# Kernel tuning notes

Hardware: AMD Instinct MI355X
Metric: run time of the kernel (lower is better)

## Reference

```python
import jax, jax.numpy as jnp
import numpy as np

# Dimensions
B, T, H = 4, 4096, 2048          # batch, seq, hidden
NH = 16                           # total hash heads = (max_ngram-1)*n_head_per_ngram
PER_HEAD_VOCAB = 100000
DH = 64                           # per-head embedding dim
E = NH * DH                       # engram_hidden_size = 1024
G = 4                             # hc_mult
K = 4                             # kernel_size
DIL = 3                           # dilation = max_ngram_size
EPS_RMS = 1.1920929e-07           # torch RMSNorm default eps (fp32 finfo eps)
EPS_SC = 1e-5                     # ShortConv RMSNorm eps


def setup_inputs() -> dict:
    key = jax.random.key(0)
    ks = jax.random.split(key, 12)
    hidden_states = jax.random.normal(ks[0], (T, B, H), dtype=jnp.float32)
    hash_ids = jax.random.randint(ks[1], (B, T, NH), 0, PER_HEAD_VOCAB)
    emb_table = jax.random.normal(ks[2], (NH * PER_HEAD_VOCAB, DH), dtype=jnp.float32)
    s = 0.02
    key_W = jax.random.normal(ks[3], (G, H, E), dtype=jnp.float32) * s
    key_b = jax.random.normal(ks[4], (G, H), dtype=jnp.float32) * s
    value_W = jax.random.normal(ks[5], (H, E), dtype=jnp.float32) * s
    value_b = jax.random.normal(ks[6], (H,), dtype=jnp.float32) * s
    norm1_w = jnp.ones((G, H), dtype=jnp.float32)
    norm2_w = jnp.ones((G, H), dtype=jnp.float32)
    sc_norm_w = jnp.ones((G, H), dtype=jnp.float32)
    conv_w = jax.random.normal(ks[7], (G * H, K), dtype=jnp.float32) * 0.1
    return {"hidden_states": hidden_states, "hash_ids": hash_ids, "emb_table": emb_table,
            "key_W": key_W, "key_b": key_b, "value_W": value_W, "value_b": value_b,
            "norm1_w": norm1_w, "norm2_w": norm2_w, "sc_norm_w": sc_norm_w, "conv_w": conv_w}


def _rms(x, eps):
    return x * jax.lax.rsqrt(jnp.mean(x * x, axis=-1, keepdims=True) + eps)


def reference(hidden_states, hash_ids, emb_table, key_W, key_b, value_W, value_b,
              norm1_w, norm2_w, sc_norm_w, conv_w):
    # --- precompute_embeddings: hashed multi-head gather ---
    offsets = jnp.arange(NH, dtype=hash_ids.dtype) * PER_HEAD_VOCAB
    emb = emb_table[hash_ids + offsets]              # [B,T,NH,DH]
    emb = emb.reshape(B, T, E)                       # [B,T,E]

    # --- forward ---
    hs = jnp.transpose(hidden_states, (1, 0, 2))     # [B,T,H]
    # per-group key projection + RMSNorm (vectorized over G)
    keys = jnp.einsum('bte,ghe->btgh', emb, key_W) + key_b   # [B,T,G,H]
    nk = _rms(keys, EPS_RMS) * norm1_w               # [B,T,G,H]
    nq = _rms(hs, EPS_RMS)[:, :, None, :] * norm2_w  # [B,T,G,H]
    gate = jnp.sum(nk * nq, axis=-1) / np.sqrt(H)    # [B,T,G]
    gate = jnp.sqrt(jnp.maximum(jnp.abs(gate), 1e-6)) * jnp.sign(gate)
    gate = jax.nn.sigmoid(gate)[..., None]           # [B,T,G,1]
    value = gate * (emb @ value_W.T + value_b)[:, :, None, :]   # [B,T,G,H]

    # --- ShortConv: per-group RMSNorm -> causal dilated depthwise conv -> SiLU ---
    xn = _rms(value, EPS_SC) * sc_norm_w             # [B,T,G,H]
    x_bct = xn.reshape(B, T, G * H).transpose(0, 2, 1)  # [B,G*H,T]
    y = jax.lax.conv_general_dilated(
        x_bct, conv_w[:, None, :],                   # rhs [C,1,K]
        window_strides=(1,), padding=[((K - 1) * DIL, 0)],
        rhs_dilation=(DIL,), dimension_numbers=('NCH', 'OIH', 'NCH'),
        feature_group_count=G * H)                   # [B,G*H,T]
    y = jax.nn.silu(y)
    y = y.transpose(0, 2, 1).reshape(B, T, G, H)

    out = (value + y).mean(axis=2)                   # [B,T,H]
    return jnp.transpose(out, (1, 0, 2))             # [S,B,H]
```

## Files before the change

### kernel.cpp

```cpp
#include <hip/hip_runtime.h>
#include <hip/hip_bf16.h>

#define BB 4
#define TT 4096
#define HH 2048
#define NHH 16
#define VOC 100000
#define EE 1024
#define GG 4
#define BT (BB*TT)
#define NKEY (GG*HH)
#define NTOT (NKEY+HH)
#define NPART 32
#define TCV 48

static constexpr float EPS_RMS = 1.1920929e-07f;
static constexpr float EPS_SC  = 1e-5f;
static constexpr float INV_SQRT_H = 0.02209708691207961f;

using f32x4 = __attribute__((ext_vector_type(4))) float;
using f32x2 = __attribute__((ext_vector_type(2))) float;
using s8v   = __attribute__((ext_vector_type(8))) short;
using gvoid = __attribute__((address_space(1))) const void;
using lvoid = __attribute__((address_space(3))) void;

__device__ __forceinline__ unsigned short f2bf(float f){
  union { __hip_bfloat16 h; unsigned short u; } cv;
  cv.h = __float2bfloat16(f);
  return cv.u;
}
__device__ __forceinline__ float bf2f(unsigned short u){
  union { float f; unsigned u; } cv;
  cv.u = ((unsigned)u) << 16;
  return cv.f;
}

__global__ __launch_bounds__(256) void convw_kern(const float* __restrict__ kW,
    const float* __restrict__ vW, unsigned short* __restrict__ Wc){
  const long idx  = (long)blockIdx.x*256 + threadIdx.x;
  const long base = idx*4;
  const long KN   = (long)NKEY*EE;
  float4 v;
  if (base < KN) v = *(const float4*)(kW + base);
  else           v = *(const float4*)(vW + (base - KN));
  ushort4 o; o.x=f2bf(v.x); o.y=f2bf(v.y); o.z=f2bf(v.z); o.w=f2bf(v.w);
  *(ushort4*)(Wc + base) = o;
}

__global__ __launch_bounds__(256) void prep_kern(const int* __restrict__ hids,
    const float* __restrict__ table, unsigned short* __restrict__ emb,
    const float* __restrict__ hs, float* __restrict__ rq,
    unsigned short* __restrict__ hsbf){
  const int p = blockIdx.x, tid = threadIdx.x;
  const int e = tid*4, head = e>>6, d = e&63;
  const long row = (long)hids[p*NHH + head] + (long)head*VOC;
  const float4 v = *(const float4*)(table + row*64 + d);
  ushort4 o; o.x=f2bf(v.x); o.y=f2bf(v.y); o.z=f2bf(v.z); o.w=f2bf(v.w);
  *(ushort4*)(emb + (size_t)p*EE + e) = o;
  const int b = p>>12, t = p&4095;
  const float* hrow = hs + ((size_t)t*BB + b)*HH;
  const int e8 = tid*8;
  float4 v0 = *(const float4*)(hrow+e8);
  float4 v1 = *(const float4*)(hrow+e8+4);
  ushort4 hb0; hb0.x=f2bf(v0.x); hb0.y=f2bf(v0.y); hb0.z=f2bf(v0.z); hb0.w=f2bf(v0.w);
  ushort4 hb1; hb1.x=f2bf(v1.x); hb1.y=f2bf(v1.y); hb1.z=f2bf(v1.z); hb1.w=f2bf(v1.w);
  *(ushort4*)(hsbf + (size_t)p*HH + e8)     = hb0;
  *(ushort4*)(hsbf + (size_t)p*HH + e8 + 4) = hb1;
  float s = v0.x*v0.x+v0.y*v0.y+v0.z*v0.z+v0.w*v0.w
          + v1.x*v1.x+v1.y*v1.y+v1.z*v1.z+v1.w*v1.w;
  #pragma unroll
  for (int of=32;of>=1;of>>=1) s += __shfl_xor(s,of);
  __shared__ float red[4];
  if ((tid&63)==0) red[tid>>6] = s;
  __syncthreads();
  if (tid==0){
    float tot = red[0]+red[1]+red[2]+red[3];
    rq[p] = rsqrtf(tot*(1.0f/HH) + EPS_RMS);
  }
}

__global__ __launch_bounds__(512, 2) void gemm8(
    const unsigned short* __restrict__ A, const unsigned short* __restrict__ Bw,
    const float* __restrict__ key_b, const float* __restrict__ value_b,
    const float* __restrict__ n1w, const float* __restrict__ n2w,
    const unsigned short* __restrict__ hsbf, unsigned short* __restrict__ vlinb,
    f32x2* __restrict__ sdp, float* __restrict__ vsqp)
{
  __shared__ unsigned short sh[65536];
  const int tid = threadIdx.x, w = tid>>6, l = tid&63;
  const int wm = w>>2, wn = w&3;
  const int lg = l&15, lr = l>>4;
  const int wg  = blockIdx.x;
  const int swz = (wg&7)*320 + (wg>>3);
  const int tM  = swz/40, tN = swz - tM*40;
  const int Mrow0 = tM*256, Nrow0 = tN*256;

  const int lp = l>>3, lcs = (l&7)^lp;
  const size_t aoffT = (size_t)(Mrow0 + w*16 + lp)*EE + lcs*8;
  const size_t boffT = (size_t)(Nrow0 + w*16 + lp)*EE + lcs*8;
  const int c0 = lr ^ (lg&7);
  const unsigned aBase = (unsigned)(wm*8192 + lg*64);
  const unsigned bBase = (unsigned)(16384 + (wn>>1)*8192 + (wn&1)*4096 + lg*64);

  f32x4 acc[8][4] = {};
  s8v aR0[4], aR1[4], bR0[4], bR1[4];

#define STAGEH(ISB, H, KT, SB) { \
    const unsigned short* s0_ = ((ISB) ? (Bw + boffT) : (A + aoffT)) + (H)*131072 + (KT)*64; \
    const unsigned d0_ = (SB)*32768 + (ISB)*16384 + (H)*8192 + w*1024; \
    __builtin_amdgcn_global_load_lds((gvoid*)s0_,        (lvoid*)(sh + d0_),       16, 0, 0); \
    __builtin_amdgcn_global_load_lds((gvoid*)(s0_+8192), (lvoid*)(sh + d0_ + 512), 16, 0, 0); \
  }
#define STAGE4(KT, SB) { STAGEH(0,0,KT,SB); STAGEH(0,1,KT,SB); STAGEH(1,0,KT,SB); STAGEH(1,1,KT,SB); }

#define BAR() { asm volatile("" ::: "memory"); __builtin_amdgcn_s_barrier(); asm volatile("" ::: "memory"); }

#define RD_A(CB, KK, MH, DST) { \
    const unsigned short* p_ = sh + (CB)*32768 + aBase; \
    const unsigned ck_ = (unsigned)((c0 ^ ((KK)<<2))<<3); \
    DST[0] = *(const s8v*)(p_ + ((MH)*4+0)*1024 + ck_); \
    DST[1] = *(const s8v*)(p_ + ((MH)*4+1)*1024 + ck_); \
    DST[2] = *(const s8v*)(p_ + ((MH)*4+2)*1024 + ck_); \
    DST[3] = *(const s8v*)(p_ + ((MH)*4+3)*1024 + ck_); }

#define RD_B(CB, KK, DST) { \
    const unsigned short* p_ = sh + (CB)*32768 + bBase; \
    const unsigned ck_ = (unsigned)((c0 ^ ((KK)<<2))<<3); \
    DST[0] = *(const s8v*)(p_ + 0*1024 + ck_); \
    DST[1] = *(const s8v*)(p_ + 1*1024 + ck_); \
    DST[2] = *(const s8v*)(p_ + 2*1024 + ck_); \
    DST[3] = *(const s8v*)(p_ + 3*1024 + ck_); }

#define MM(MH, AF, BF) { \
    __builtin_amdgcn_s_setprio(1); \
    _Pragma("unroll") \
    for (int mf=0; mf<4; mf++) \
      _Pragma("unroll") \
      for (int nf=0; nf<4; nf++) \
        acc[(MH)*4+mf][nf] = __builtin_amdgcn_mfma_f32_16x16x32_bf16(AF[mf], BF[nf], acc[(MH)*4+mf][nf], 0,0,0); \
    __builtin_amdgcn_s_setprio(0); }

#define TILE(CB, NB, KT1, DOST) { \
    BAR(); \
    if (DOST) STAGE4(KT1, NB); \
    RD_A(CB,1,0,aR1); RD_B(CB,1,bR1); \
    MM(0, aR0, bR0); \
    RD_A(CB,0,1,aR0); \
    MM(0, aR1, bR1); \
    RD_A(CB,1,1,aR1); \
    MM(1, aR0, bR0); \
    asm volatile("s_waitcnt vmcnt(0)" ::: "memory"); \
    BAR(); \
    RD_A(NB,0,0,aR0); RD_B(NB,0,bR0); \
    MM(1, aR1, bR1); }

#define TILE_LAST(CB) { \
    BAR(); \
    RD_A(CB,1,0,aR1); RD_B(CB,1,bR1); \
    MM(0, aR0, bR0); \
    RD_A(CB,0,1,aR0); \
    MM(0, aR1, bR1); \
    RD_A(CB,1,1,aR1); \
    MM(1, aR0, bR0); \
    MM(1, aR1, bR1); }

  STAGE4(0, 0);
  asm volatile("s_waitcnt vmcnt(0)" ::: "memory");
  BAR();
  RD_A(0,0,0,aR0); RD_B(0,0,bR0);

  #pragma unroll 1
  for (int i=0; i<7; i++){
    const int kt = 2*i;
    TILE(0, 1, kt+1, true);
    TILE(1, 0, kt+2, true);
  }
  TILE(0, 1, 15, true);
  TILE_LAST(1);

#undef STAGEH
#undef STAGE4
#undef RD_A
#undef RD_B
#undef MM
#undef TILE
#undef TILE_LAST

  BAR();

  const bool isK = (Nrow0 < NKEY);
  float bias[4], cw[4]; int hcol[4];
  #pragma unroll
  for (int nf=0; nf<4; nf++){
    const int n = Nrow0 + wn*64 + nf*16 + lg;
    hcol[nf] = n & (HH-1);
    if (isK){ bias[nf] = key_b[n]; cw[nf] = n1w[n]*n2w[n]; }
    else    { bias[nf] = value_b[n-NKEY]; cw[nf] = 0.f; }
  }

  if (isK){
    const int g = Nrow0 >> 11;
    const int slot = (tN&7)*4 + wn;
    char* wreg = (char*)sh + w*16384;
    #pragma unroll
    for (int mfa=0; mfa<8; mfa++){
      #pragma unroll
      for (int rr=0; rr<4; rr++){
        const int rowl = mfa*16 + lr*4 + rr;
        const int p = Mrow0 + wm*128 + rowl;
        const unsigned short* hrow = hsbf + (size_t)p*HH;
        float ssq=0.f, dt=0.f;
        #pragma unroll
        for (int nf=0; nf<4; nf++){
          const float c = acc[mfa][nf][rr] + bias[nf];
          ssq += c*c;
          dt  += c * cw[nf] * bf2f(hrow[hcol[nf]]);
        }
        f32x2 pr; pr[0]=ssq; pr[1]=dt;
        *(f32x2*)(wreg + rowl*128 + (((lg>>1) ^ (rowl&7))<<4) + ((lg&1)<<3)) = pr;
      }
    }
    #pragma unroll
    for (int rh=0; rh<2; rh++){
      const int r = l + rh*64;
      float ssq=0.f, dt=0.f;
      #pragma unroll
      for (int c=0; c<8; c++){
        f32x4 v = *(const f32x4*)(wreg + r*128 + ((c ^ (r&7))<<4));
        ssq += v[0] + v[2]; dt += v[1] + v[3];
      }
      const int p = Mrow0 + wm*128 + r;
      f32x2 o; o[0]=ssq; o[1]=dt;
      sdp[(size_t)(p*GG+g)*NPART + slot] = o;
    }
  } else {
    const int slot = (tN-32)*4 + wn;
    const int h0 = Nrow0 - NKEY + wn*64;
    const int pbase = Mrow0 + wm*128;
    #pragma unroll
    for (int mfa=0; mfa<8; mfa++){
      #pragma unroll
      for (int rr=0; rr<4; rr++){
        const int p = pbase + mfa*16 + lr*4 + rr;
        float ssq=0.f;
        #pragma unroll
        for (int nf=0; nf<4; nf++){
          const float c = acc[mfa][nf][rr] + bias[nf];
          vlinb[(size_t)p*HH + h0 + nf*16 + lg] = f2bf(c);
          ssq += c*c;
        }
        #pragma unroll
        for (int o=1;o<16;o<<=1){ ssq += __shfl_xor(ssq,o); }
        if (lg==0) vsqp[(size_t)p*NPART + slot] = ssq;
      }
    }
  }
}

__global__ __launch_bounds__(256) void scal_kern(const f32x2* __restrict__ sdp,
    const float* __restrict__ vsqp,
    const float* __restrict__ rq, float* __restrict__ gate, float* __restrict__ av){
  const int i = blockIdx.x*256 + threadIdx.x;
  const int p = i>>2;
  float ss=0.f, dd=0.f, vv=0.f;
  const f32x2* sp = sdp + (size_t)i*NPART;
  #pragma unroll
  for (int j=0;j<NPART;j++){ f32x2 v = sp[j]; ss += v[0]; dd += v[1]; }
  #pragma unroll
  for (int j=0;j<NPART;j++){ vv += vsqp[(size_t)p*NPART+j]; }
  const float rk = rsqrtf(ss*(1.0f/HH) + EPS_RMS);
  const float gv = rk * rq[p] * dd * INV_SQRT_H;
  const float sgn = (gv>0.f)?1.f:((gv<0.f)?-1.f:0.f);
  const float g1 = sqrtf(fmaxf(fabsf(gv),1e-6f))*sgn;
  const float gt = 1.f/(1.f+__expf(-g1));
  const float msvl = vv*(1.0f/HH);
  const float a = gt * rsqrtf(gt*gt*msvl + EPS_SC);
  gate[i]=gt; av[i]=a;
}

__device__ __forceinline__ ushort4 ldrow(const unsigned short* __restrict__ v, int b, int t, int h0){
  if (t < 0){ ushort4 z; z.x=0;z.y=0;z.z=0;z.w=0; return z; }
  return *(const ushort4*)(v + (size_t)((b<<12)|t)*HH + h0);
}
__device__ __forceinline__ void ldav(const float* __restrict__ av, int b, int t, float* a){
  if (t < 0){ a[0]=0.f;a[1]=0.f;a[2]=0.f;a[3]=0.f; }
  else { const float4 x = *(const float4*)(av + (size_t)((b<<12)|t)*GG);
         a[0]=x.x;a[1]=x.y;a[2]=x.z;a[3]=x.w; }
}

__global__ __launch_bounds__(256) void conv2_kern(const unsigned short* __restrict__ vlinb,
    const float* __restrict__ gate, const float* __restrict__ av,
    const float* __restrict__ conv_w, const float* __restrict__ scw,
    float* __restrict__ out){
  const int bx = blockIdx.x;
  const int b  = blockIdx.y;
  const int t0 = (bx>>1)*TCV;
  const int h0 = (bx&1)*1024 + threadIdx.x*4;

  float cwv[4][4][4];
  float sc4[4][4];
  #pragma unroll
  for (int g=0; g<4; g++){
    #pragma unroll
    for (int j2=0; j2<4; j2++){
      const int c = g*HH + h0 + j2;
      const float4 wv = *(const float4*)(conv_w + (size_t)c*4);
      cwv[g][j2][0]=wv.x; cwv[g][j2][1]=wv.y; cwv[g][j2][2]=wv.z; cwv[g][j2][3]=wv.w;
      sc4[g][j2] = scw[c];
    }
  }

  #pragma unroll 1
  for (int r=0; r<3; r++){
    const int tf = t0 + r;
    ushort4 w0 = ldrow(vlinb, b, tf-9, h0);
    ushort4 w1 = ldrow(vlinb, b, tf-6, h0);
    ushort4 w2 = ldrow(vlinb, b, tf-3, h0);
    ushort4 w3; w3.x=0;w3.y=0;w3.z=0;w3.w=0;
    #pragma unroll
    for (int j=0; j<16; j++){
      const int t = tf + 3*j;
      if (t < TT){
        const int p = (b<<12)|t;
        w3 = *(const ushort4*)(vlinb + (size_t)p*HH + h0);
        float a0[4],a1[4],a2[4],a3[4];
        ldav(av, b, t-9, a0); ldav(av, b, t-6, a1); ldav(av, b, t-3, a2); ldav(av, b, t, a3);
        float gt4[4];
        { const float4 x = *(const float4*)(gate + (size_t)p*GG);
          gt4[0]=x.x; gt4[1]=x.y; gt4[2]=x.z; gt4[3]=x.w; }
        float v0[4],v1[4],v2[4],v3[4];
        v0[0]=bf2f(w0.x); v0[1]=bf2f(w0.y); v0[2]=bf2f(w0.z); v0[3]=bf2f(w0.w);
        v1[0]=bf2f(w1.x); v1[1]=bf2f(w1.y); v1[2]=bf2f(w1.z); v1[3]=bf2f(w1.w);
        v2[0]=bf2f(w2.x); v2[1]=bf2f(w2.y); v2[2]=bf2f(w2.z); v2[3]=bf2f(w2.w);
        v3[0]=bf2f(w3.x); v3[1]=bf2f(w3.y); v3[2]=bf2f(w3.z); v3[3]=bf2f(w3.w);
        float4 ov;
        float res[4];
        #pragma unroll
        for (int j2=0; j2<4; j2++){
          float acc = 0.f;
          #pragma unroll
          for (int g=0; g<4; g++){
            float y = cwv[g][j2][0]*a0[g]*v0[j2]
                    + cwv[g][j2][1]*a1[g]*v1[j2]
                    + cwv[g][j2][2]*a2[g]*v2[j2]
                    + cwv[g][j2][3]*a3[g]*v3[j2];
            y *= sc4[g][j2];
            const float sy = y * (1.f/(1.f+__expf(-y)));
            acc += gt4[g]*v3[j2] + sy;
          }
          res[j2] = acc*0.25f;
        }
        ov.x=res[0]; ov.y=res[1]; ov.z=res[2]; ov.w=res[3];
        *(float4*)(out + ((size_t)t*BB + b)*HH + h0) = ov;
      }
      w0=w1; w1=w2; w2=w3;
    }
  }
}

extern "C" void kernel_launch(void* const* d_in, const int* in_sizes, int n_in,
                              void* d_out, int out_size, void* d_ws, size_t ws_size,
                              hipStream_t stream){
  (void)in_sizes; (void)n_in; (void)out_size; (void)ws_size;
  const float* hs    = (const float*)d_in[0];
  const int*   hids  = (const int*)d_in[1];
  const float* table = (const float*)d_in[2];
  const float* keyW  = (const float*)d_in[3];
  const float* keyB  = (const float*)d_in[4];
  const float* valW  = (const float*)d_in[5];
  const float* valB  = (const float*)d_in[6];
  const float* n1w   = (const float*)d_in[7];
  const float* n2w   = (const float*)d_in[8];
  const float* scw   = (const float*)d_in[9];
  const float* convw = (const float*)d_in[10];
  float* out = (float*)d_out;

  char* ws = (char*)d_ws;
  size_t off = 0;
  unsigned short* emb   = (unsigned short*)(ws+off); off += (size_t)BT*EE*2;
  unsigned short* Wc    = (unsigned short*)(ws+off); off += (size_t)NTOT*EE*2;
  unsigned short* vlinb = (unsigned short*)(ws+off); off += (size_t)BT*HH*2;
  unsigned short* hsbf  = (unsigned short*)(ws+off); off += (size_t)BT*HH*2;
  f32x2* sdp    = (f32x2*)(ws+off); off += (size_t)BT*GG*NPART*8;
  float* vsqp   = (float*)(ws+off); off += (size_t)BT*NPART*4;
  float* rq     = (float*)(ws+off); off += (size_t)BT*4;
  float* gate   = (float*)(ws+off); off += (size_t)BT*GG*4;
  float* av     = (float*)(ws+off); off += (size_t)BT*GG*4;

  convw_kern<<<(NTOT*EE/4)/256, 256, 0, stream>>>(keyW, valW, Wc);
  prep_kern<<<BT, 256, 0, stream>>>(hids, table, emb, hs, rq, hsbf);
  gemm8<<<2560, 512, 0, stream>>>(emb, Wc, keyB, valB, n1w, n2w, hsbf, vlinb, sdp, vsqp);
  scal_kern<<<(BT*GG)/256, 256, 0, stream>>>(sdp, vsqp, rq, gate, av);
  dim3 cg(((TT + TCV - 1)/TCV)*2, BB);
  conv2_kern<<<cg, 256, 0, stream>>>(vlinb, gate, av, convw, scw, out);
}
```

Baseline: 554.5 us.

## Pre-pack GEMM operands into MFMA fragment layout and load directly to registers

The weight cast and the embedding gather now write A and B in a fragment-major layout. Each lane can then fetch its 16-byte MFMA fragment straight from global memory. This lets the GEMM drop LDS staging, the swizzled LDS reads and the barriers, and use a simple register double-buffered loop. The tile-to-block mapping also changes to a new stripe-based swizzle for L2 locality. The cost is that every wave reissues global loads with no LDS sharing, so the kernel leans more on L2 bandwidth and latency hiding from two blocks per CU. The 128KB LDS array is still reserved for the epilogue.

```diff
diff --git a/kernel.cpp b/kernel.cpp
--- a/kernel.cpp
+++ b/kernel.cpp
@@ -21,8 +21,6 @@
 using f32x4 = __attribute__((ext_vector_type(4))) float;
 using f32x2 = __attribute__((ext_vector_type(2))) float;
 using s8v   = __attribute__((ext_vector_type(8))) short;
-using gvoid = __attribute__((address_space(1))) const void;
-using lvoid = __attribute__((address_space(3))) void;
 
 __device__ __forceinline__ unsigned short f2bf(float f){
   union { __hip_bfloat16 h; unsigned short u; } cv;
@@ -34,38 +32,56 @@
   cv.u = ((unsigned)u) << 16;
   return cv.f;
 }
-
-__global__ __launch_bounds__(256) void convw_kern(const float* __restrict__ kW,
-    const float* __restrict__ vW, unsigned short* __restrict__ Wc){
-  const long idx  = (long)blockIdx.x*256 + threadIdx.x;
-  const long base = idx*4;
-  const long KN   = (long)NKEY*EE;
-  float4 v;
-  if (base < KN) v = *(const float4*)(kW + base);
-  else           v = *(const float4*)(vW + (base - KN));
-  ushort4 o; o.x=f2bf(v.x); o.y=f2bf(v.y); o.z=f2bf(v.z); o.w=f2bf(v.w);
-  *(ushort4*)(Wc + base) = o;
-}
-
-__global__ __launch_bounds__(256) void prep_kern(const int* __restrict__ hids,
-    const float* __restrict__ table, unsigned short* __restrict__ emb,
-    const float* __restrict__ hs, float* __restrict__ rq,
-    unsigned short* __restrict__ hsbf){
+__device__ __forceinline__ s8v pack8(float4 v0, float4 v1){
+  s8v o;
+  o[0]=(short)f2bf(v0.x); o[1]=(short)f2bf(v0.y); o[2]=(short)f2bf(v0.z); o[3]=(short)f2bf(v0.w);
+  o[4]=(short)f2bf(v1.x); o[5]=(short)f2bf(v1.y); o[6]=(short)f2bf(v1.z); o[7]=(short)f2bf(v1.w);
+  return o;
+}
+
+__global__ __launch_bounds__(256) void convw_pack(const float* __restrict__ kW,
+    const float* __restrict__ vW, unsigned short* __restrict__ Bpk){
+  const int nb = blockIdx.x;
+  const int t = threadIdx.x, lane = t&63, q = t>>6;
+  const int n = nb*16 + (lane&15);
+  const float* src = (n < NKEY) ? (kW + (size_t)n*EE) : (vW + (size_t)(n-NKEY)*EE);
+  #pragma unroll
+  for (int i=0;i<8;i++){
+    const int kb = q*8 + i;
+    const int k0 = kb*32 + (lane>>4)*8;
+    float4 v0 = *(const float4*)(src + k0);
+    float4 v1 = *(const float4*)(src + k0 + 4);
+    *(s8v*)(Bpk + (size_t)(nb*32 + kb)*512 + lane*8) = pack8(v0, v1);
+  }
+}
+
+__global__ __launch_bounds__(256) void prep_pack(const int* __restrict__ hids,
+    const float* __restrict__ table, unsigned short* __restrict__ Apk){
+  const int pb = blockIdx.x;
+  const int t = threadIdx.x, lane = t&63, q = t>>6;
+  const int p = pb*16 + (lane&15);
+  #pragma unroll
+  for (int i=0;i<8;i++){
+    const int kb = q*8 + i;
+    const int k0 = kb*32 + (lane>>4)*8;
+    const int head = k0>>6;
+    const long row = (long)hids[p*NHH + head] + (long)head*VOC;
+    const float* src = table + row*64 + (k0&63);
+    float4 v0 = *(const float4*)(src);
+    float4 v1 = *(const float4*)(src + 4);
+    *(s8v*)(Apk + (size_t)(pb*32 + kb)*512 + lane*8) = pack8(v0, v1);
+  }
+}
+
+__global__ __launch_bounds__(256) void prep_hs(const float* __restrict__ hs,
+    float* __restrict__ rq, unsigned short* __restrict__ hsbf){
   const int p = blockIdx.x, tid = threadIdx.x;
-  const int e = tid*4, head = e>>6, d = e&63;
-  const long row = (long)hids[p*NHH + head] + (long)head*VOC;
-  const float4 v = *(const float4*)(table + row*64 + d);
-  ushort4 o; o.x=f2bf(v.x); o.y=f2bf(v.y); o.z=f2bf(v.z); o.w=f2bf(v.w);
-  *(ushort4*)(emb + (size_t)p*EE + e) = o;
   const int b = p>>12, t = p&4095;
   const float* hrow = hs + ((size_t)t*BB + b)*HH;
   const int e8 = tid*8;
   float4 v0 = *(const float4*)(hrow+e8);
   float4 v1 = *(const float4*)(hrow+e8+4);
-  ushort4 hb0; hb0.x=f2bf(v0.x); hb0.y=f2bf(v0.y); hb0.z=f2bf(v0.z); hb0.w=f2bf(v0.w);
-  ushort4 hb1; hb1.x=f2bf(v1.x); hb1.y=f2bf(v1.y); hb1.z=f2bf(v1.z); hb1.w=f2bf(v1.w);
-  *(ushort4*)(hsbf + (size_t)p*HH + e8)     = hb0;
-  *(ushort4*)(hsbf + (size_t)p*HH + e8 + 4) = hb1;
+  *(s8v*)(hsbf + (size_t)p*HH + e8) = pack8(v0, v1);
   float s = v0.x*v0.x+v0.y*v0.y+v0.z*v0.z+v0.w*v0.w
           + v1.x*v1.x+v1.y*v1.y+v1.z*v1.z+v1.w*v1.w;
   #pragma unroll
@@ -79,114 +95,58 @@
   }
 }
 
-__global__ __launch_bounds__(512, 2) void gemm8(
-    const unsigned short* __restrict__ A, const unsigned short* __restrict__ Bw,
+__global__ __launch_bounds__(512, 2) void gemm(
+    const unsigned short* __restrict__ Apk, const unsigned short* __restrict__ Bpk,
     const float* __restrict__ key_b, const float* __restrict__ value_b,
     const float* __restrict__ n1w, const float* __restrict__ n2w,
     const unsigned short* __restrict__ hsbf, unsigned short* __restrict__ vlinb,
     f32x2* __restrict__ sdp, float* __restrict__ vsqp)
 {
-  __shared__ unsigned short sh[65536];
+  __shared__ char sh[131072];
   const int tid = threadIdx.x, w = tid>>6, l = tid&63;
   const int wm = w>>2, wn = w&3;
   const int lg = l&15, lr = l>>4;
-  const int wg  = blockIdx.x;
-  const int swz = (wg&7)*320 + (wg>>3);
-  const int tM  = swz/40, tN = swz - tM*40;
+  const int wg = blockIdx.x;
+  const int x = wg&7, lid = wg>>3;
+  const int stripe = lid/160, rr0 = lid - stripe*160;
+  const int tN = rr0>>2, tM = x*8 + stripe*4 + (rr0&3);
   const int Mrow0 = tM*256, Nrow0 = tN*256;
 
-  const int lp = l>>3, lcs = (l&7)^lp;
-  const size_t aoffT = (size_t)(Mrow0 + w*16 + lp)*EE + lcs*8;
-  const size_t boffT = (size_t)(Nrow0 + w*16 + lp)*EE + lcs*8;
-  const int c0 = lr ^ (lg&7);
-  const unsigned aBase = (unsigned)(wm*8192 + lg*64);
-  const unsigned bBase = (unsigned)(16384 + (wn>>1)*8192 + (wn&1)*4096 + lg*64);
+  unsigned aof[8], bof[4];
+  #pragma unroll
+  for (int mf=0;mf<8;mf++) aof[mf] = (unsigned)((tM*16 + wm*8 + mf)*32)*512u + (unsigned)l*8u;
+  #pragma unroll
+  for (int nf=0;nf<4;nf++) bof[nf] = (unsigned)((tN*16 + wn*4 + nf)*32)*512u + (unsigned)l*8u;
 
   f32x4 acc[8][4] = {};
-  s8v aR0[4], aR1[4], bR0[4], bR1[4];
-
-#define STAGEH(ISB, H, KT, SB) { \
-    const unsigned short* s0_ = ((ISB) ? (Bw + boffT) : (A + aoffT)) + (H)*131072 + (KT)*64; \
-    const unsigned d0_ = (SB)*32768 + (ISB)*16384 + (H)*8192 + w*1024; \
-    __builtin_amdgcn_global_load_lds((gvoid*)s0_,        (lvoid*)(sh + d0_),       16, 0, 0); \
-    __builtin_amdgcn_global_load_lds((gvoid*)(s0_+8192), (lvoid*)(sh + d0_ + 512), 16, 0, 0); \
-  }
-#define STAGE4(KT, SB) { STAGEH(0,0,KT,SB); STAGEH(0,1,KT,SB); STAGEH(1,0,KT,SB); STAGEH(1,1,KT,SB); }
-
-#define BAR() { asm volatile("" ::: "memory"); __builtin_amdgcn_s_barrier(); asm volatile("" ::: "memory"); }
-
-#define RD_A(CB, KK, MH, DST) { \
-    const unsigned short* p_ = sh + (CB)*32768 + aBase; \
-    const unsigned ck_ = (unsigned)((c0 ^ ((KK)<<2))<<3); \
-    DST[0] = *(const s8v*)(p_ + ((MH)*4+0)*1024 + ck_); \
-    DST[1] = *(const s8v*)(p_ + ((MH)*4+1)*1024 + ck_); \
-    DST[2] = *(const s8v*)(p_ + ((MH)*4+2)*1024 + ck_); \
-    DST[3] = *(const s8v*)(p_ + ((MH)*4+3)*1024 + ck_); }
-
-#define RD_B(CB, KK, DST) { \
-    const unsigned short* p_ = sh + (CB)*32768 + bBase; \
-    const unsigned ck_ = (unsigned)((c0 ^ ((KK)<<2))<<3); \
-    DST[0] = *(const s8v*)(p_ + 0*1024 + ck_); \
-    DST[1] = *(const s8v*)(p_ + 1*1024 + ck_); \
-    DST[2] = *(const s8v*)(p_ + 2*1024 + ck_); \
-    DST[3] = *(const s8v*)(p_ + 3*1024 + ck_); }
-
-#define MM(MH, AF, BF) { \
+  s8v aA[8], aB[8], bA[4], bB[4];
+
+#define LDF(DSTA, DSTB, S) { \
+    _Pragma("unroll") \
+    for (int mf_=0;mf_<8;mf_++) DSTA[mf_] = *(const s8v*)(Apk + aof[mf_] + (unsigned)(S)*512u); \
+    _Pragma("unroll") \
+    for (int nf_=0;nf_<4;nf_++) DSTB[nf_] = *(const s8v*)(Bpk + bof[nf_] + (unsigned)(S)*512u); }
+
+#define MMB(AF, BF) { \
     __builtin_amdgcn_s_setprio(1); \
     _Pragma("unroll") \
-    for (int mf=0; mf<4; mf++) \
+    for (int mf_=0;mf_<8;mf_++) \
       _Pragma("unroll") \
-      for (int nf=0; nf<4; nf++) \
-        acc[(MH)*4+mf][nf] = __builtin_amdgcn_mfma_f32_16x16x32_bf16(AF[mf], BF[nf], acc[(MH)*4+mf][nf], 0,0,0); \
+      for (int nf_=0;nf_<4;nf_++) \
+        acc[mf_][nf_] = __builtin_amdgcn_mfma_f32_16x16x32_bf16(AF[mf_], BF[nf_], acc[mf_][nf_], 0,0,0); \
     __builtin_amdgcn_s_setprio(0); }
 
-#define TILE(CB, NB, KT1, DOST) { \
-    BAR(); \
-    if (DOST) STAGE4(KT1, NB); \
-    RD_A(CB,1,0,aR1); RD_B(CB,1,bR1); \
-    MM(0, aR0, bR0); \
-    RD_A(CB,0,1,aR0); \
-    MM(0, aR1, bR1); \
-    RD_A(CB,1,1,aR1); \
-    MM(1, aR0, bR0); \
-    asm volatile("s_waitcnt vmcnt(0)" ::: "memory"); \
-    BAR(); \
-    RD_A(NB,0,0,aR0); RD_B(NB,0,bR0); \
-    MM(1, aR1, bR1); }
-
-#define TILE_LAST(CB) { \
-    BAR(); \
-    RD_A(CB,1,0,aR1); RD_B(CB,1,bR1); \
-    MM(0, aR0, bR0); \
-    RD_A(CB,0,1,aR0); \
-    MM(0, aR1, bR1); \
-    RD_A(CB,1,1,aR1); \
-    MM(1, aR0, bR0); \
-    MM(1, aR1, bR1); }
-
-  STAGE4(0, 0);
-  asm volatile("s_waitcnt vmcnt(0)" ::: "memory");
-  BAR();
-  RD_A(0,0,0,aR0); RD_B(0,0,bR0);
-
+  LDF(aA, bA, 0);
   #pragma unroll 1
-  for (int i=0; i<7; i++){
-    const int kt = 2*i;
-    TILE(0, 1, kt+1, true);
-    TILE(1, 0, kt+2, true);
-  }
-  TILE(0, 1, 15, true);
-  TILE_LAST(1);
-
-#undef STAGEH
-#undef STAGE4
-#undef RD_A
-#undef RD_B
-#undef MM
-#undef TILE
-#undef TILE_LAST
-
-  BAR();
+  for (int s=0; s<32; s+=2){
+    LDF(aB, bB, s+1);
+    MMB(aA, bA);
+    const int s2 = (s+2 < 32) ? s+2 : 31;
+    LDF(aA, bA, s2);
+    MMB(aB, bB);
+  }
+#undef LDF
+#undef MMB
 
   const bool isK = (Nrow0 < NKEY);
   float bias[4], cw[4]; int hcol[4];
@@ -201,7 +161,7 @@
   if (isK){
     const int g = Nrow0 >> 11;
     const int slot = (tN&7)*4 + wn;
-    char* wreg = (char*)sh + w*16384;
+    char* wreg = sh + w*16384;
     #pragma unroll
     for (int mfa=0; mfa<8; mfa++){
       #pragma unroll
@@ -326,8 +286,8 @@
         float a0[4],a1[4],a2[4],a3[4];
         ldav(av, b, t-9, a0); ldav(av, b, t-6, a1); ldav(av, b, t-3, a2); ldav(av, b, t, a3);
         float gt4[4];
-        { const float4 x = *(const float4*)(gate + (size_t)p*GG);
-          gt4[0]=x.x; gt4[1]=x.y; gt4[2]=x.z; gt4[3]=x.w; }
+        { const float4 xx = *(const float4*)(gate + (size_t)p*GG);
+          gt4[0]=xx.x; gt4[1]=xx.y; gt4[2]=xx.z; gt4[3]=xx.w; }
         float v0[4],v1[4],v2[4],v3[4];
         v0[0]=bf2f(w0.x); v0[1]=bf2f(w0.y); v0[2]=bf2f(w0.z); v0[3]=bf2f(w0.w);
         v1[0]=bf2f(w1.x); v1[1]=bf2f(w1.y); v1[2]=bf2f(w1.z); v1[3]=bf2f(w1.w);
@@ -377,8 +337,8 @@
 
   char* ws = (char*)d_ws;
   size_t off = 0;
-  unsigned short* emb   = (unsigned short*)(ws+off); off += (size_t)BT*EE*2;
-  unsigned short* Wc    = (unsigned short*)(ws+off); off += (size_t)NTOT*EE*2;
+  unsigned short* Apk   = (unsigned short*)(ws+off); off += (size_t)BT*EE*2;
+  unsigned short* Bpk   = (unsigned short*)(ws+off); off += (size_t)NTOT*EE*2;
   unsigned short* vlinb = (unsigned short*)(ws+off); off += (size_t)BT*HH*2;
   unsigned short* hsbf  = (unsigned short*)(ws+off); off += (size_t)BT*HH*2;
   f32x2* sdp    = (f32x2*)(ws+off); off += (size_t)BT*GG*NPART*8;
@@ -387,9 +347,10 @@
   float* gate   = (float*)(ws+off); off += (size_t)BT*GG*4;
   float* av     = (float*)(ws+off); off += (size_t)BT*GG*4;
 
-  convw_kern<<<(NTOT*EE/4)/256, 256, 0, stream>>>(keyW, valW, Wc);
-  prep_kern<<<BT, 256, 0, stream>>>(hids, table, emb, hs, rq, hsbf);
-  gemm8<<<2560, 512, 0, stream>>>(emb, Wc, keyB, valB, n1w, n2w, hsbf, vlinb, sdp, vsqp);
+  convw_pack<<<NTOT/16, 256, 0, stream>>>(keyW, valW, Bpk);
+  prep_pack<<<BT/16, 256, 0, stream>>>(hids, table, Apk);
+  prep_hs<<<BT, 256, 0, stream>>>(hs, rq, hsbf);
+  gemm<<<2560, 512, 0, stream>>>(Apk, Bpk, keyB, valB, n1w, n2w, hsbf, vlinb, sdp, vsqp);
   scal_kern<<<(BT*GG)/256, 256, 0, stream>>>(sdp, vsqp, rq, gate, av);
   dim3 cg(((TT + TCV - 1)/TCV)*2, BB);
   conv2_kern<<<cg, 256, 0, stream>>>(vlinb, gate, av, convw, scw, out);
```

After: 697.4 us. 1.26x slower.

## Triple-buffer GEMM LDS pipeline with half-depth K tiles and rolling conv scale registers

Applied to the files above, without the earlier changes.

The bf16 MFMA GEMM main loop moves from a double-buffered 64-wide K tile to a triple-buffered 32-wide K tile. Two stages are prefetched ahead and waits use a partial vmcnt, so global-to-LDS loads overlap more MFMA work. LDS is enlarged to 96KB and the swizzle and fragment read layout are reworked, which may reduce occupancy at 2 blocks per CU. The key epilogue is split into two halves to fit the smaller per-wave scratch. The conv kernel keeps the scale factors for earlier timesteps in registers and rotates them instead of reloading four per step.

```diff
diff --git a/kernel.cpp b/kernel.cpp
--- a/kernel.cpp
+++ b/kernel.cpp
@@ -86,7 +86,7 @@
     const unsigned short* __restrict__ hsbf, unsigned short* __restrict__ vlinb,
     f32x2* __restrict__ sdp, float* __restrict__ vsqp)
 {
-  __shared__ unsigned short sh[65536];
+  __shared__ char sh[98304];
   const int tid = threadIdx.x, w = tid>>6, l = tid&63;
   const int wm = w>>2, wn = w&3;
   const int lg = l&15, lr = l>>4;
@@ -95,98 +95,96 @@
   const int tM  = swz/40, tN = swz - tM*40;
   const int Mrow0 = tM*256, Nrow0 = tN*256;
 
-  const int lp = l>>3, lcs = (l&7)^lp;
-  const size_t aoffT = (size_t)(Mrow0 + w*16 + lp)*EE + lcs*8;
-  const size_t boffT = (size_t)(Nrow0 + w*16 + lp)*EE + lcs*8;
-  const int c0 = lr ^ (lg&7);
-  const unsigned aBase = (unsigned)(wm*8192 + lg*64);
-  const unsigned bBase = (unsigned)(16384 + (wn>>1)*8192 + (wn&1)*4096 + lg*64);
+  const int srow = l>>2, schunk = (l&3) ^ (srow&3);
+  const size_t aoffS = (size_t)(Mrow0 + w*32 + srow)*EE + schunk*8;
+  const size_t boffS = (size_t)(Nrow0 + w*32 + srow)*EE + schunk*8;
+  const unsigned cSw = (unsigned)((lr ^ (lg&3))<<4);
+  const unsigned aB0 = (unsigned)(wm*8192 + lg*64) + cSw;
+  const unsigned bB0 = 16384u + (unsigned)(wn*4096 + lg*64) + cSw;
 
   f32x4 acc[8][4] = {};
-  s8v aR0[4], aR1[4], bR0[4], bR1[4];
-
-#define STAGEH(ISB, H, KT, SB) { \
-    const unsigned short* s0_ = ((ISB) ? (Bw + boffT) : (A + aoffT)) + (H)*131072 + (KT)*64; \
-    const unsigned d0_ = (SB)*32768 + (ISB)*16384 + (H)*8192 + w*1024; \
-    __builtin_amdgcn_global_load_lds((gvoid*)s0_,        (lvoid*)(sh + d0_),       16, 0, 0); \
-    __builtin_amdgcn_global_load_lds((gvoid*)(s0_+8192), (lvoid*)(sh + d0_ + 512), 16, 0, 0); \
-  }
-#define STAGE4(KT, SB) { STAGEH(0,0,KT,SB); STAGEH(0,1,KT,SB); STAGEH(1,0,KT,SB); STAGEH(1,1,KT,SB); }
+  s8v aF0, aF1, aR2, aR3, aR4, aR5, aR6, aR7;
+  s8v bP[4], bQ[4];
 
 #define BAR() { asm volatile("" ::: "memory"); __builtin_amdgcn_s_barrier(); asm volatile("" ::: "memory"); }
-
-#define RD_A(CB, KK, MH, DST) { \
-    const unsigned short* p_ = sh + (CB)*32768 + aBase; \
-    const unsigned ck_ = (unsigned)((c0 ^ ((KK)<<2))<<3); \
-    DST[0] = *(const s8v*)(p_ + ((MH)*4+0)*1024 + ck_); \
-    DST[1] = *(const s8v*)(p_ + ((MH)*4+1)*1024 + ck_); \
-    DST[2] = *(const s8v*)(p_ + ((MH)*4+2)*1024 + ck_); \
-    DST[3] = *(const s8v*)(p_ + ((MH)*4+3)*1024 + ck_); }
-
-#define RD_B(CB, KK, DST) { \
-    const unsigned short* p_ = sh + (CB)*32768 + bBase; \
-    const unsigned ck_ = (unsigned)((c0 ^ ((KK)<<2))<<3); \
-    DST[0] = *(const s8v*)(p_ + 0*1024 + ck_); \
-    DST[1] = *(const s8v*)(p_ + 1*1024 + ck_); \
-    DST[2] = *(const s8v*)(p_ + 2*1024 + ck_); \
-    DST[3] = *(const s8v*)(p_ + 3*1024 + ck_); }
-
-#define MM(MH, AF, BF) { \
+#define WAITV(N) asm volatile("s_waitcnt vmcnt(" #N ")" ::: "memory")
+
+#define STG(ISB, J, KT, SB) { \
+    const unsigned short* s_ = ((ISB) ? (Bw + boffS) : (A + aoffS)) + (J)*16*EE + (KT)*32; \
+    __builtin_amdgcn_global_load_lds((gvoid*)s_, \
+        (lvoid*)(sh + (SB)*32768 + (ISB)*16384 + w*2048 + (J)*1024), 16, 0, 0); }
+#define STAGE4(KT, SB) { STG(0,0,KT,SB); STG(0,1,KT,SB); STG(1,0,KT,SB); STG(1,1,KT,SB); }
+
+#define RD_A(CB, MF, DST) { DST = *(const s8v*)(sh + (CB)*32768 + aB0 + (MF)*1024); }
+#define RD_B(CB, DSTARR) { \
+    DSTARR[0] = *(const s8v*)(sh + (CB)*32768 + bB0 + 0*1024); \
+    DSTARR[1] = *(const s8v*)(sh + (CB)*32768 + bB0 + 1*1024); \
+    DSTARR[2] = *(const s8v*)(sh + (CB)*32768 + bB0 + 2*1024); \
+    DSTARR[3] = *(const s8v*)(sh + (CB)*32768 + bB0 + 3*1024); }
+
+#define MM4(MF, AF, BF) { \
     __builtin_amdgcn_s_setprio(1); \
-    _Pragma("unroll") \
-    for (int mf=0; mf<4; mf++) \
-      _Pragma("unroll") \
-      for (int nf=0; nf<4; nf++) \
-        acc[(MH)*4+mf][nf] = __builtin_amdgcn_mfma_f32_16x16x32_bf16(AF[mf], BF[nf], acc[(MH)*4+mf][nf], 0,0,0); \
+    acc[MF][0] = __builtin_amdgcn_mfma_f32_16x16x32_bf16(AF, BF[0], acc[MF][0], 0,0,0); \
+    acc[MF][1] = __builtin_amdgcn_mfma_f32_16x16x32_bf16(AF, BF[1], acc[MF][1], 0,0,0); \
+    acc[MF][2] = __builtin_amdgcn_mfma_f32_16x16x32_bf16(AF, BF[2], acc[MF][2], 0,0,0); \
+    acc[MF][3] = __builtin_amdgcn_mfma_f32_16x16x32_bf16(AF, BF[3], acc[MF][3], 0,0,0); \
     __builtin_amdgcn_s_setprio(0); }
 
-#define TILE(CB, NB, KT1, DOST) { \
+#define TILEX(CB, NB, SB, KT2, BC, BN, DOST, WMACRO) { \
     BAR(); \
-    if (DOST) STAGE4(KT1, NB); \
-    RD_A(CB,1,0,aR1); RD_B(CB,1,bR1); \
-    MM(0, aR0, bR0); \
-    RD_A(CB,0,1,aR0); \
-    MM(0, aR1, bR1); \
-    RD_A(CB,1,1,aR1); \
-    MM(1, aR0, bR0); \
-    asm volatile("s_waitcnt vmcnt(0)" ::: "memory"); \
+    if (DOST) STAGE4(KT2, SB); \
+    RD_A(CB,2,aR2); RD_A(CB,3,aR3); \
+    MM4(0, aF0, BC); \
+    RD_A(CB,4,aR4); RD_A(CB,5,aR5); \
+    MM4(1, aF1, BC); \
+    RD_A(CB,6,aR6); RD_A(CB,7,aR7); \
+    MM4(2, aR2, BC); MM4(3, aR3, BC); \
+    WMACRO; \
     BAR(); \
-    RD_A(NB,0,0,aR0); RD_B(NB,0,bR0); \
-    MM(1, aR1, bR1); }
-
-#define TILE_LAST(CB) { \
+    MM4(4, aR4, BC); MM4(5, aR5, BC); \
+    RD_A(NB,0,aF0); RD_A(NB,1,aF1); RD_B(NB, BN); \
+    MM4(6, aR6, BC); MM4(7, aR7, BC); }
+
+#define TILE_FIN(CB, BC) { \
     BAR(); \
-    RD_A(CB,1,0,aR1); RD_B(CB,1,bR1); \
-    MM(0, aR0, bR0); \
-    RD_A(CB,0,1,aR0); \
-    MM(0, aR1, bR1); \
-    RD_A(CB,1,1,aR1); \
-    MM(1, aR0, bR0); \
-    MM(1, aR1, bR1); }
+    RD_A(CB,2,aR2); RD_A(CB,3,aR3); \
+    MM4(0, aF0, BC); \
+    RD_A(CB,4,aR4); RD_A(CB,5,aR5); \
+    MM4(1, aF1, BC); \
+    RD_A(CB,6,aR6); RD_A(CB,7,aR7); \
+    MM4(2, aR2, BC); MM4(3, aR3, BC); MM4(4, aR4, BC); MM4(5, aR5, BC); \
+    MM4(6, aR6, BC); MM4(7, aR7, BC); }
 
   STAGE4(0, 0);
-  asm volatile("s_waitcnt vmcnt(0)" ::: "memory");
+  STAGE4(1, 1);
+  WAITV(4);
   BAR();
-  RD_A(0,0,0,aR0); RD_B(0,0,bR0);
+  RD_A(0,0,aF0); RD_A(0,1,aF1); RD_B(0, bP);
 
   #pragma unroll 1
-  for (int i=0; i<7; i++){
-    const int kt = 2*i;
-    TILE(0, 1, kt+1, true);
-    TILE(1, 0, kt+2, true);
-  }
-  TILE(0, 1, 15, true);
-  TILE_LAST(1);
-
-#undef STAGEH
+  for (int i=0; i<5; i++){
+    const int k6 = 6*i;
+    TILEX(0,1,2, k6+2, bP,bQ, 1, WAITV(4));
+    TILEX(1,2,0, k6+3, bQ,bP, 1, WAITV(4));
+    TILEX(2,0,1, k6+4, bP,bQ, 1, WAITV(4));
+    TILEX(0,1,2, k6+5, bQ,bP, 1, WAITV(4));
+    TILEX(1,2,0, k6+6, bP,bQ, 1, WAITV(4));
+    TILEX(2,0,1, k6+7, bQ,bP, 1, WAITV(4));
+  }
+  TILEX(0,1,2, 0, bP,bQ, 0, WAITV(0));
+  TILE_FIN(1, bQ);
+
+#undef BAR
+#undef WAITV
+#undef STG
 #undef STAGE4
 #undef RD_A
 #undef RD_B
-#undef MM
-#undef TILE
-#undef TILE_LAST
-
-  BAR();
+#undef MM4
+#undef TILEX
+#undef TILE_FIN
+
+  asm volatile("" ::: "memory"); __builtin_amdgcn_s_barrier(); asm volatile("" ::: "memory");
 
   const bool isK = (Nrow0 < NKEY);
   float bias[4], cw[4]; int hcol[4];
@@ -201,37 +199,40 @@
   if (isK){
     const int g = Nrow0 >> 11;
     const int slot = (tN&7)*4 + wn;
-    char* wreg = (char*)sh + w*16384;
+    char* wreg = sh + w*8192;
     #pragma unroll
-    for (int mfa=0; mfa<8; mfa++){
+    for (int half=0; half<2; half++){
       #pragma unroll
-      for (int rr=0; rr<4; rr++){
-        const int rowl = mfa*16 + lr*4 + rr;
-        const int p = Mrow0 + wm*128 + rowl;
-        const unsigned short* hrow = hsbf + (size_t)p*HH;
+      for (int mfs=0; mfs<4; mfs++){
+        const int mfa = half*4 + mfs;
+        #pragma unroll
+        for (int rr=0; rr<4; rr++){
+          const int rowl2 = mfs*16 + lr*4 + rr;
+          const int p = Mrow0 + wm*128 + half*64 + rowl2;
+          const unsigned short* hrow = hsbf + (size_t)p*HH;
+          float ssq=0.f, dt=0.f;
+          #pragma unroll
+          for (int nf=0; nf<4; nf++){
+            const float c = acc[mfa][nf][rr] + bias[nf];
+            ssq += c*c;
+            dt  += c * cw[nf] * bf2f(hrow[hcol[nf]]);
+          }
+          f32x2 pr; pr[0]=ssq; pr[1]=dt;
+          *(f32x2*)(wreg + rowl2*128 + (((lg>>1) ^ (rowl2&7))<<4) + ((lg&1)<<3)) = pr;
+        }
+      }
+      {
+        const int r = l;
         float ssq=0.f, dt=0.f;
         #pragma unroll
-        for (int nf=0; nf<4; nf++){
-          const float c = acc[mfa][nf][rr] + bias[nf];
-          ssq += c*c;
-          dt  += c * cw[nf] * bf2f(hrow[hcol[nf]]);
+        for (int c=0; c<8; c++){
+          f32x4 v = *(const f32x4*)(wreg + r*128 + ((c ^ (r&7))<<4));
+          ssq += v[0] + v[2]; dt += v[1] + v[3];
         }
-        f32x2 pr; pr[0]=ssq; pr[1]=dt;
-        *(f32x2*)(wreg + rowl*128 + (((lg>>1) ^ (rowl&7))<<4) + ((lg&1)<<3)) = pr;
+        const int p = Mrow0 + wm*128 + half*64 + r;
+        f32x2 o; o[0]=ssq; o[1]=dt;
+        sdp[(size_t)(p*GG+g)*NPART + slot] = o;
       }
-    }
-    #pragma unroll
-    for (int rh=0; rh<2; rh++){
-      const int r = l + rh*64;
-      float ssq=0.f, dt=0.f;
-      #pragma unroll
-      for (int c=0; c<8; c++){
-        f32x4 v = *(const f32x4*)(wreg + r*128 + ((c ^ (r&7))<<4));
-        ssq += v[0] + v[2]; dt += v[1] + v[3];
-      }
-      const int p = Mrow0 + wm*128 + r;
-      f32x2 o; o[0]=ssq; o[1]=dt;
-      sdp[(size_t)(p*GG+g)*NPART + slot] = o;
     }
   } else {
     const int slot = (tN-32)*4 + wn;
@@ -317,17 +318,18 @@
     ushort4 w1 = ldrow(vlinb, b, tf-6, h0);
     ushort4 w2 = ldrow(vlinb, b, tf-3, h0);
     ushort4 w3; w3.x=0;w3.y=0;w3.z=0;w3.w=0;
+    float a0[4],a1[4],a2[4],a3[4];
+    ldav(av, b, tf-9, a0); ldav(av, b, tf-6, a1); ldav(av, b, tf-3, a2);
     #pragma unroll
     for (int j=0; j<16; j++){
       const int t = tf + 3*j;
       if (t < TT){
         const int p = (b<<12)|t;
         w3 = *(const ushort4*)(vlinb + (size_t)p*HH + h0);
-        float a0[4],a1[4],a2[4],a3[4];
-        ldav(av, b, t-9, a0); ldav(av, b, t-6, a1); ldav(av, b, t-3, a2); ldav(av, b, t, a3);
+        ldav(av, b, t, a3);
         float gt4[4];
-        { const float4 x = *(const float4*)(gate + (size_t)p*GG);
-          gt4[0]=x.x; gt4[1]=x.y; gt4[2]=x.z; gt4[3]=x.w; }
+        { const float4 xx = *(const float4*)(gate + (size_t)p*GG);
+          gt4[0]=xx.x; gt4[1]=xx.y; gt4[2]=xx.z; gt4[3]=xx.w; }
         float v0[4],v1[4],v2[4],v3[4];
         v0[0]=bf2f(w0.x); v0[1]=bf2f(w0.y); v0[2]=bf2f(w0.z); v0[3]=bf2f(w0.w);
         v1[0]=bf2f(w1.x); v1[1]=bf2f(w1.y); v1[2]=bf2f(w1.z); v1[3]=bf2f(w1.w);
@@ -354,6 +356,8 @@
         *(float4*)(out + ((size_t)t*BB + b)*HH + h0) = ov;
       }
       w0=w1; w1=w2; w2=w3;
+      #pragma unroll
+      for (int g=0; g<4; g++){ a0[g]=a1[g]; a1[g]=a2[g]; a2[g]=a3[g]; }
     }
   }
 }
```

Measured after the change: 569.5 us. +2.7%, slower.
